# Optimization experiments

Hardware: AMD Instinct MI355X
Metric: run time of the kernel (lower is better)

Reference implementation:

```python
import jax, jax.numpy as jnp
import numpy as np

B, C, H, W = 8, 96, 160, 320
MH, MW = 4, 4

def setup_inputs() -> dict:
    key = jax.random.key(0)
    k1, k2 = jax.random.split(key)
    feat1 = jax.random.normal(k1, (B, C, H, W), dtype=jnp.float32)
    feat2 = jax.random.normal(k2, (B, C, H, W), dtype=jnp.float32)
    return {"feat1": feat1, "feat2": feat2, "max_offset_h": MH, "max_offset_w": MW}

def reference(feat1, feat2, max_offset_h, max_offset_w):
    # feat1, feat2: [B, C, H, W]
    # cost[b, d, h, w] = sum_c feat1[b,c,h,w] * feat2[b,c,h+dh,w+dw]
    # with (dh, dw) enumerating the (2*mh+1)*(2*mw+1) offset window and
    # zero padding outside image boundaries.
    b, c, h, w = feat1.shape
    mh, mw = max_offset_h, max_offset_w
    padded = jnp.pad(feat2, ((0, 0), (0, 0), (mh, mh), (mw, mw)))
    costs = []
    for dh in range(2 * mh + 1):
        for dw in range(2 * mw + 1):
            shifted = jax.lax.dynamic_slice(padded, (0, 0, dh, dw), (b, c, h, w))
            costs.append(jnp.sum(feat1 * shifted, axis=1))  # [B, H, W]
    return jnp.stack(costs, axis=1)  # [B, (2mh+1)*(2mw+1), H, W]
```

## Files before the change

kernel.cpp:

```cpp
#include <hip/hip_runtime.h>

#define B_   8
#define C_   96
#define H_   160
#define W_   320
#define ND   9
#define NDD  81
#define TH   16
#define TW   16
#define KC   3
#define NCH  32
#define F2ROWS 18
#define F2STRIDE 24
#define F2PLANE (F2ROWS*F2STRIDE)
#define BUFW (KC*F2PLANE)
#define LDSWORDS 5376

#define AS1 __attribute__((address_space(1)))
#define AS3 __attribute__((address_space(3)))

__device__ __forceinline__ void gld16(const float* gp, float* lp) {
    __builtin_amdgcn_global_load_lds((const AS1 float*)gp,
                                     (AS3 float*)(unsigned long long)lp, 16, 0, 0);
}

__global__ __launch_bounds__(192, 4)
void corr_kernel(const float* __restrict__ f1g,
                 const float* __restrict__ f2g,
                 float* __restrict__ out)
{
    __shared__ float lds[LDSWORDS];

    const int tid  = threadIdx.x;
    const int wave = tid >> 6;
    const int lane = tid & 63;
    const int row  = lane >> 2;
    const int colb = (lane & 3) << 2;

    const int bid  = blockIdx.x;
    const int ebid = (bid & 7) * 600 + (bid >> 3);
    const int b    = ebid / 600;
    const int t6   = ebid - b * 600;
    const int g    = t6 % 3;
    const int tile = t6 / 3;
    const int by   = tile / 20, bx = tile - by * 20;
    const int x0 = bx * TW, y0 = by * TH;
    const int HWi  = H_ * W_;
    const int r0   = y0 + 3 * g - 4;

    const float* f1b = f1g + (size_t)b * C_ * HWi;
    const float* f2b = f2g + (size_t)b * C_ * HWi;

    const float* f1p = f1b + (y0 + row) * W_ + x0 + colb;

    int so0, so1; bool p0, p1;
    {
        int s, r, c, gy, gx;
        s = lane;      r = s / 6; c = (s - 6 * r) << 2;
        gy = r0 + r;   gx = x0 - 4 + c;
        p0 = (gy >= 0) & (gy < H_) & (gx >= 0) & (gx <= W_ - 4);
        so0 = gy * W_ + gx;
        s = 64 + lane; r = s / 6; c = (s - 6 * r) << 2;
        gy = r0 + r;   gx = x0 - 4 + c;
        p1 = (s < 108) & (gy >= 0) & (gy < H_) & (gx >= 0) & (gx <= W_ - 4);
        so1 = gy * W_ + gx;
    }

    const int o0 = (row + wave) * F2STRIDE + colb;

    auto stage = [&](int cb, int bufb) {
        const int co = (cb + wave) * HWi;
        float* l = &lds[bufb + wave * F2PLANE];
        if (p0) gld16(f2b + co + so0, l);
        if (p1) gld16(f2b + co + so1, l + 256);
    };

    float4 acc0, acc1, acc2, acc3, acc4, acc5, acc6, acc7, acc8;
    acc0 = acc1 = acc2 = acc3 = acc4 = acc5 = acc6 = acc7 = acc8 = make_float4(0.f, 0.f, 0.f, 0.f);
    float4 P0, P1, P2;

#define F1LOAD(cb) {                                         \
        P0 = *(const float4*)(f1p + (cb) * HWi);             \
        P1 = *(const float4*)(f1p + ((cb) + 1) * HWi);       \
        P2 = *(const float4*)(f1p + ((cb) + 2) * HWi); }

#define STEPD(A, P, e0, e1, e2, e3)                          \
        A.x = fmaf(P.x, e0, A.x);                            \
        A.y = fmaf(P.y, e1, A.y);                            \
        A.z = fmaf(P.z, e2, A.z);                            \
        A.w = fmaf(P.w, e3, A.w);

#define COMPC(c, RB, P) {                                                         \
        const float4 q0 = *(const float4*)&lds[(RB) + c * F2PLANE + o0];          \
        const float4 q1 = *(const float4*)&lds[(RB) + c * F2PLANE + o0 + 4];      \
        const float4 q2 = *(const float4*)&lds[(RB) + c * F2PLANE + o0 + 8];      \
        STEPD(acc0, P, q0.x, q0.y, q0.z, q0.w)                                    \
        STEPD(acc1, P, q0.y, q0.z, q0.w, q1.x)                                    \
        STEPD(acc2, P, q0.z, q0.w, q1.x, q1.y)                                    \
        STEPD(acc3, P, q0.w, q1.x, q1.y, q1.z)                                    \
        STEPD(acc4, P, q1.x, q1.y, q1.z, q1.w)                                    \
        STEPD(acc5, P, q1.y, q1.z, q1.w, q2.x)                                    \
        STEPD(acc6, P, q1.z, q1.w, q2.x, q2.y)                                    \
        STEPD(acc7, P, q1.w, q2.x, q2.y, q2.z)                                    \
        STEPD(acc8, P, q2.x, q2.y, q2.z, q2.w)                                    \
    }

    for (int t = tid; t < LDSWORDS; t += 192) lds[t] = 0.f;
    __syncthreads();
    stage(0, 0);

#pragma unroll 1
    for (int kk = 0; kk < NCH / 2; ++kk) {
        const int c0 = 6 * kk;
        __syncthreads();
        F1LOAD(c0)
        stage(c0 + 3, BUFW);
        COMPC(0, 0, P0) COMPC(1, 0, P1) COMPC(2, 0, P2)
        __syncthreads();
        F1LOAD(c0 + 3)
        if (kk < NCH / 2 - 1) stage(c0 + 6, 0);
        COMPC(0, BUFW, P0) COMPC(1, BUFW, P1) COMPC(2, BUFW, P2)
    }

    const int dh = 3 * g + wave;
    const int gy = y0 + row;
    const int gx = x0 + colb;
#define STORED(d) {                                                                 \
        float* op_ = out + (size_t)((b * NDD + dh * ND + d) * H_ + gy) * W_ + gx;   \
        *(float4*)op_ = acc##d; }
    STORED(0) STORED(1) STORED(2) STORED(3) STORED(4)
    STORED(5) STORED(6) STORED(7) STORED(8)
}

extern "C" void kernel_launch(void* const* d_in, const int* in_sizes, int n_in,
                              void* d_out, int out_size, void* d_ws, size_t ws_size,
                              hipStream_t stream)
{
    const float* f1 = (const float*)d_in[0];
    const float* f2 = (const float*)d_in[1];
    float* out = (float*)d_out;
    corr_kernel<<<dim3(4800), 192, 0, stream>>>(f1, f2, out);
}
```

Baseline: 214.7 us.

## Triple-buffer feat2 staging with 6-channel chunks and explicit vmcnt waits

Restructures the channel loop into 16 chunks of 6 channels with three LDS buffers, prefetching two chunks ahead. It replaces __syncthreads with manual s_waitcnt vmcnt plus s_barrier, and adds sched_barriers to fix the instruction order. The LDS row stride is padded from 24 to 28 to cut bank conflicts. LDS use grows and launch bounds drop to 2 blocks per CU, trading occupancy for deeper latency hiding and fewer barriers. Correctness now depends on the hand-counted vmcnt value, which also counts the feat1 global loads.

```diff
diff --git a/kernel.cpp b/kernel.cpp
--- a/kernel.cpp
+++ b/kernel.cpp
@@ -8,13 +8,14 @@
 #define NDD  81
 #define TH   16
 #define TW   16
-#define KC   3
-#define NCH  32
+#define KC   6
+#define NCH  16
 #define F2ROWS 18
-#define F2STRIDE 24
+#define F2STRIDE 28
 #define F2PLANE (F2ROWS*F2STRIDE)
 #define BUFW (KC*F2PLANE)
-#define LDSWORDS 5376
+#define NBUF 3
+#define LDSWORDS (NBUF*BUFW)
 
 #define AS1 __attribute__((address_space(1)))
 #define AS3 __attribute__((address_space(3)))
@@ -24,7 +25,7 @@
                                      (AS3 float*)(unsigned long long)lp, 16, 0, 0);
 }
 
-__global__ __launch_bounds__(192, 4)
+__global__ __launch_bounds__(192, 2)
 void corr_kernel(const float* __restrict__ f1g,
                  const float* __restrict__ f2g,
                  float* __restrict__ out)
@@ -56,33 +57,40 @@
     int so0, so1; bool p0, p1;
     {
         int s, r, c, gy, gx;
-        s = lane;      r = s / 6; c = (s - 6 * r) << 2;
+        s = lane;      r = s / 7; c = (s - 7 * r) << 2;
         gy = r0 + r;   gx = x0 - 4 + c;
-        p0 = (gy >= 0) & (gy < H_) & (gx >= 0) & (gx <= W_ - 4);
+        p0 = (c < 24) & (gy >= 0) & (gy < H_) & (gx >= 0) & (gx <= W_ - 4);
         so0 = gy * W_ + gx;
-        s = 64 + lane; r = s / 6; c = (s - 6 * r) << 2;
+        s = 64 + lane; r = s / 7; c = (s - 7 * r) << 2;
         gy = r0 + r;   gx = x0 - 4 + c;
-        p1 = (s < 108) & (gy >= 0) & (gy < H_) & (gx >= 0) & (gx <= W_ - 4);
+        p1 = (s < 126) & (c < 24) & (gy >= 0) & (gy < H_) & (gx >= 0) & (gx <= W_ - 4);
         so1 = gy * W_ + gx;
     }
 
     const int o0 = (row + wave) * F2STRIDE + colb;
 
     auto stage = [&](int cb, int bufb) {
-        const int co = (cb + wave) * HWi;
-        float* l = &lds[bufb + wave * F2PLANE];
-        if (p0) gld16(f2b + co + so0, l);
-        if (p1) gld16(f2b + co + so1, l + 256);
+#pragma unroll
+        for (int j = 0; j < 2; ++j) {
+            const int ch = 3 * j + wave;
+            const int co = (cb + ch) * HWi;
+            float* l = &lds[bufb + ch * F2PLANE];
+            if (p0) gld16(f2b + co + so0, l);
+            if (p1) gld16(f2b + co + so1, l + 256);
+        }
     };
 
     float4 acc0, acc1, acc2, acc3, acc4, acc5, acc6, acc7, acc8;
     acc0 = acc1 = acc2 = acc3 = acc4 = acc5 = acc6 = acc7 = acc8 = make_float4(0.f, 0.f, 0.f, 0.f);
-    float4 P0, P1, P2;
+    float4 P0, P1, P2, P3, P4, P5;
 
 #define F1LOAD(cb) {                                         \
         P0 = *(const float4*)(f1p + (cb) * HWi);             \
         P1 = *(const float4*)(f1p + ((cb) + 1) * HWi);       \
-        P2 = *(const float4*)(f1p + ((cb) + 2) * HWi); }
+        P2 = *(const float4*)(f1p + ((cb) + 2) * HWi);       \
+        P3 = *(const float4*)(f1p + ((cb) + 3) * HWi);       \
+        P4 = *(const float4*)(f1p + ((cb) + 4) * HWi);       \
+        P5 = *(const float4*)(f1p + ((cb) + 5) * HWi); }
 
 #define STEPD(A, P, e0, e1, e2, e3)                          \
         A.x = fmaf(P.x, e0, A.x);                            \
@@ -104,22 +112,27 @@
         STEPD(acc7, P, q1.w, q2.x, q2.y, q2.z)                                    \
         STEPD(acc8, P, q2.x, q2.y, q2.z, q2.w)                                    \
     }
+#define CHUNK(RB) COMPC(0,RB,P0) COMPC(1,RB,P1) COMPC(2,RB,P2) \
+                  COMPC(3,RB,P3) COMPC(4,RB,P4) COMPC(5,RB,P5)
 
     for (int t = tid; t < LDSWORDS; t += 192) lds[t] = 0.f;
     __syncthreads();
+
     stage(0, 0);
+    stage(KC, BUFW);
 
 #pragma unroll 1
-    for (int kk = 0; kk < NCH / 2; ++kk) {
-        const int c0 = 6 * kk;
-        __syncthreads();
-        F1LOAD(c0)
-        stage(c0 + 3, BUFW);
-        COMPC(0, 0, P0) COMPC(1, 0, P1) COMPC(2, 0, P2)
-        __syncthreads();
-        F1LOAD(c0 + 3)
-        if (kk < NCH / 2 - 1) stage(c0 + 6, 0);
-        COMPC(0, BUFW, P0) COMPC(1, BUFW, P1) COMPC(2, BUFW, P2)
+    for (int k = 0; k < NCH; ++k) {
+        if (k < NCH - 1) { asm volatile("s_waitcnt vmcnt(4)" ::: "memory"); }
+        else             { asm volatile("s_waitcnt vmcnt(0)" ::: "memory"); }
+        __builtin_amdgcn_s_barrier();
+        __builtin_amdgcn_sched_barrier(0);
+        F1LOAD(KC * k)
+        __builtin_amdgcn_sched_barrier(0);
+        if (k + 2 < NCH) stage(KC * (k + 2), ((k + 2) % NBUF) * BUFW);
+        __builtin_amdgcn_sched_barrier(0);
+        const int rb_ = (k % NBUF) * BUFW;
+        CHUNK(rb_)
     }
 
     const int dh = 3 * g + wave;
```

Measured after the change: 216.7 us. About the same (+0.9%).
